# Performance work log

Hardware: AMD Instinct MI355X
Metric: run time of the kernel (lower is better)

## Reference

```python
import jax, jax.numpy as jnp
import numpy as np

BS, NQ, NC, NT = 64, 300, 10, 30
W_CLASS, W_BBOX, W_GIOU = 2.0, 5.0, 2.0


def cxcywh_to_xyxy(b):
    c, s = b[..., :2], b[..., 2:]
    return jnp.concatenate([c - 0.5 * s, c + 0.5 * s], axis=-1)


def _area(b):
    return (b[..., 2] - b[..., 0]) * (b[..., 3] - b[..., 1])


def giou_pairwise(a, b):
    # a: [N,4] xyxy, b: [M,4] xyxy -> [N,M]
    sum_area = _area(a)[:, None] + _area(b)[None, :]
    lt = jnp.maximum(a[:, None, :2], b[None, :, :2])
    rb = jnp.minimum(a[:, None, 2:], b[None, :, 2:])
    wh = jnp.clip(rb - lt, 0.0)
    inter = wh[..., 0] * wh[..., 1]
    union = sum_area - inter
    iou = inter / union
    ltc = jnp.minimum(a[:, None, :2], b[None, :, :2])
    rbc = jnp.maximum(a[:, None, 2:], b[None, :, 2:])
    whc = jnp.clip(rbc - ltc, 0.0)
    areac = whc[..., 0] * whc[..., 1]
    return iou - (areac - union) / areac


def giou_elementwise(a, b):
    # a, b: [N,4] xyxy -> [N]
    sum_area = _area(a) + _area(b)
    lt = jnp.maximum(a[..., :2], b[..., :2])
    rb = jnp.minimum(a[..., 2:], b[..., 2:])
    wh = jnp.clip(rb - lt, 0.0)
    inter = wh[..., 0] * wh[..., 1]
    union = sum_area - inter
    iou = inter / union
    ltc = jnp.minimum(a[..., :2], b[..., :2])
    rbc = jnp.maximum(a[..., 2:], b[..., 2:])
    whc = jnp.clip(rbc - ltc, 0.0)
    areac = whc[..., 0] * whc[..., 1]
    return iou - (areac - union) / areac


def hungarian(cost):
    # Exact rectangular assignment (Kuhn-Munkres with potentials), rows n <= cols m.
    # Returns (row_ind, col_ind) of the n matched pairs, equivalent to
    # scipy.optimize.linear_sum_assignment.
    n, m = cost.shape
    u = np.zeros(n + 1)
    v = np.zeros(m + 1)
    p = np.zeros(m + 1, dtype=np.int64)    # p[j] = row matched to col j (1-based)
    way = np.zeros(m + 1, dtype=np.int64)
    for i in range(1, n + 1):
        p[0] = i
        j0 = 0
        minv = np.full(m + 1, np.inf)
        used = np.zeros(m + 1, dtype=bool)
        while True:
            used[j0] = True
            i0 = p[j0]
            cur = cost[i0 - 1] - u[i0] - v[1:]
            mask = ~used[1:]
            better = mask & (cur < minv[1:])
            minv[1:] = np.where(better, cur, minv[1:])
            way[1:] = np.where(better, j0, way[1:])
            free = np.nonzero(mask)[0]
            j1 = free[np.argmin(minv[1:][free])] + 1
            delta = minv[j1]
            u[p[used]] += delta
            v[used] -= delta
            minv[~used] -= delta
            j0 = j1
            if p[j0] == 0:
                break
        while j0 != 0:
            j1 = way[j0]
            p[j0] = p[j1]
            j0 = j1
    rows = p[1:] - 1
    cols = np.arange(m)
    sel = rows >= 0
    return rows[sel], cols[sel]


def compute_match(pred_logits, pred_boxes, labels, boxes):
    # Mirrors @torch.no_grad() match(): build cost matrix on device, assign on host.
    bs, nq, _ = pred_logits.shape
    t = boxes.shape[1]
    out_prob = jax.nn.sigmoid(pred_logits).reshape(bs * nq, -1)
    out_bbox = pred_boxes.reshape(bs * nq, 4)
    tgt_ids = labels.reshape(-1)
    tgt_bbox = boxes.reshape(-1, 4)
    cost_class = -out_prob[:, tgt_ids]                                   # [bs*nq, bs*t]
    cost_bbox = jnp.sum(jnp.abs(out_bbox[:, None, :] - tgt_bbox[None, :, :]), -1)
    cost_giou = -giou_pairwise(cxcywh_to_xyxy(out_bbox), cxcywh_to_xyxy(tgt_bbox))
    C = W_BBOX * cost_bbox + W_CLASS * cost_class + W_GIOU * cost_giou
    C = np.asarray(jax.device_get(C), dtype=np.float64).reshape(bs, nq, bs * t)
    bidx, sidx, tidx = [], [], []
    for b in range(bs):
        block = C[b, :, b * t:(b + 1) * t]          # [nq, t]
        r, c = hungarian(block.T)                   # rows = targets, cols = queries
        bidx.extend([b] * len(c))
        sidx.extend(c.tolist())
        tidx.extend(r.tolist())
    return (np.asarray(bidx, np.int64), np.asarray(sidx, np.int64),
            np.asarray(tidx, np.int64))


def compute_loss(pred_logits, pred_boxes, labels, boxes, bidx, sidx, tidx):
    bs, nq, _ = pred_logits.shape
    num = max(1, len(bidx))
    target_classes = jnp.full((bs, nq), 10, dtype=jnp.int32)
    target_classes = target_classes.at[bidx, sidx].set(
        labels[bidx, tidx].astype(jnp.int32))
    onehot = jax.nn.one_hot(target_classes, 11, dtype=pred_logits.dtype)[..., :10]
    # sigmoid focal loss, alpha=0.25, gamma=2, reduction='sum'
    x, t = pred_logits, onehot
    p = jax.nn.sigmoid(x)
    ce = jnp.maximum(x, 0.0) - x * t + jnp.log1p(jnp.exp(-jnp.abs(x)))
    p_t = p * t + (1.0 - p) * (1.0 - t)
    alpha_t = 0.25 * t + 0.75 * (1.0 - t)
    loss_ce = jnp.sum(alpha_t * ce * (1.0 - p_t) ** 2) / num
    src_boxes = pred_boxes[bidx, sidx]
    tgt_boxes = boxes[bidx, tidx]
    loss_bbox = jnp.sum(jnp.abs(src_boxes - tgt_boxes)) / num
    g = giou_elementwise(cxcywh_to_xyxy(src_boxes), cxcywh_to_xyxy(tgt_boxes))
    loss_giou = jnp.sum(1.0 - g) / num
    return loss_ce + 5.0 * loss_bbox + 2.0 * loss_giou


def setup_inputs() -> dict:
    key = jax.random.key(0)
    k0, k1, k2, k3 = jax.random.split(key, 4)
    pred_logits = jax.random.normal(k0, (BS, NQ, NC), dtype=jnp.float32)
    pred_boxes = jax.random.uniform(k1, (BS, NQ, 4), dtype=jnp.float32)
    labels = jax.random.randint(k2, (BS, NT), 0, 10, dtype=jnp.int64)
    boxes = jax.random.uniform(k3, (BS, NT, 4), dtype=jnp.float32)
    return {"pred_logits": pred_logits, "pred_boxes": pred_boxes,
            "labels": labels, "boxes": boxes}


def reference(pred_logits, pred_boxes, labels, boxes):
    bidx, sidx, tidx = compute_match(pred_logits, pred_boxes, labels, boxes)
    return compute_loss(pred_logits, pred_boxes, labels, boxes, bidx, sidx, tidx)
```

## Files before the change

### kernel.cpp

```cpp
#include <hip/hip_runtime.h>
#include <math.h>

#define NQ 300
#define NQP 301
#define NT 30
#define NC 10
#define NTH 512
#define NWAVE 8
#define INFF 3.0e38f

__device__ __forceinline__ float sigf(float x){ return 1.0f/(1.0f + expf(-x)); }
__device__ __forceinline__ float softplusf(float x){ return fmaxf(x,0.0f) + log1pf(expf(-fabsf(x))); }
__device__ __forceinline__ float readlane_f(float v, int l){
  return __int_as_float(__builtin_amdgcn_readlane(__float_as_int(v), l));
}
__device__ __forceinline__ int readlane_i(int v, int l){
  return __builtin_amdgcn_readlane(v, l);
}

template<int CTRL,int RMASK>
__device__ __forceinline__ float dppmin_f(float x){
  int t = __builtin_amdgcn_update_dpp(0x7f800000, __float_as_int(x), CTRL, RMASK, 0xf, false);
  return fminf(x, __int_as_float(t));
}
template<int CTRL,int RMASK>
__device__ __forceinline__ unsigned dppmin_u(unsigned x){
  unsigned t = (unsigned)__builtin_amdgcn_update_dpp((int)0xFFFFFFFFu, (int)x, CTRL, RMASK, 0xf, false);
  return x < t ? x : t;
}
template<int CTRL,int RMASK>
__device__ __forceinline__ float dppadd_f(float x){
  int t = __builtin_amdgcn_update_dpp(0, __float_as_int(x), CTRL, RMASK, 0xf, false);
  return x + __int_as_float(t);
}
__device__ __forceinline__ void wave_argmin64(float v, unsigned idx, float &ov, int &oj){
  float x = v;
  x = dppmin_f<0x111,0xf>(x); x = dppmin_f<0x112,0xf>(x);
  x = dppmin_f<0x114,0xf>(x); x = dppmin_f<0x118,0xf>(x);
  x = dppmin_f<0x142,0xa>(x); x = dppmin_f<0x143,0xc>(x);
  float vmin = __int_as_float(__builtin_amdgcn_readlane(__float_as_int(x), 63));
  unsigned c = (v == vmin) ? idx : 0xFFFFFFFFu;
  c = dppmin_u<0x111,0xf>(c); c = dppmin_u<0x112,0xf>(c);
  c = dppmin_u<0x114,0xf>(c); c = dppmin_u<0x118,0xf>(c);
  c = dppmin_u<0x142,0xa>(c); c = dppmin_u<0x143,0xc>(c);
  oj = __builtin_amdgcn_readlane((int)c, 63);
  ov = vmin;
}
__device__ __forceinline__ float wave_sum64(float v){
  float x = v;
  x = dppadd_f<0x111,0xf>(x); x = dppadd_f<0x112,0xf>(x);
  x = dppadd_f<0x114,0xf>(x); x = dppadd_f<0x118,0xf>(x);
  x = dppadd_f<0x142,0xa>(x); x = dppadd_f<0x143,0xc>(x);
  return __int_as_float(__builtin_amdgcn_readlane(__float_as_int(x), 63));
}

__global__ __launch_bounds__(NTH) void hm_main(
    const float* __restrict__ logits,
    const float* __restrict__ pbox,
    const int*   __restrict__ labels,
    const float* __restrict__ tbox,
    float* __restrict__ out)
{
  const int b = blockIdx.x;
  const int tid = threadIdx.x;
  const int wv = tid >> 6, ln = tid & 63;

  __shared__ float D[NT*NQ];
  __shared__ float psmT[NC*NQP];
  __shared__ float traw[NT][4], txy[NT][4], tarea[NT];
  __shared__ int   tlab[NT];
  __shared__ float uu[NT+1];
  __shared__ int   pcol[NQ];
  __shared__ int   claimA[NQ];
  __shared__ int   rargm[NT];
  __shared__ float redw[NWAVE];

  const bool v4 = ln < (NQ - 256);

  float qcx[5],qcy[5],qw[5],qh[5],qx0[5],qy0[5],qx1[5],qy1[5],qar[5];
  {
    const float4* pb4 = (const float4*)pbox + (size_t)b*NQ;
    #pragma unroll
    for (int k = 0; k < 5; ++k) {
      float4 s = (k < 4 || v4) ? pb4[ln + (k<<6)] : make_float4(0.f,0.f,0.f,0.f);
      qcx[k]=s.x; qcy[k]=s.y; qw[k]=s.z; qh[k]=s.w;
      qx0[k]=s.x-0.5f*s.z; qy0[k]=s.y-0.5f*s.w;
      qx1[k]=s.x+0.5f*s.z; qy1[k]=s.y+0.5f*s.w;
      qar[k]=(qx1[k]-qx0[k])*(qy1[k]-qy0[k]);
    }
  }
  if (tid < NT) {
    float4 s = ((const float4*)tbox)[(size_t)b*NT + tid];
    traw[tid][0]=s.x; traw[tid][1]=s.y; traw[tid][2]=s.z; traw[tid][3]=s.w;
    float x0=s.x-0.5f*s.z, y0=s.y-0.5f*s.w, x1=s.x+0.5f*s.z, y1=s.y+0.5f*s.w;
    txy[tid][0]=x0; txy[tid][1]=y0; txy[tid][2]=x1; txy[tid][3]=y1;
    tarea[tid]=(x1-x0)*(y1-y0);
    tlab[tid]=labels[b*NT + tid];
  }
  for (int j = tid; j < NQ; j += NTH) { pcol[j]=0; claimA[j]=0x7fffffff; }

  float tot = 0.f;
  for (int e = tid; e < NQ*NC; e += NTH) {
    float x = logits[(size_t)b*NQ*NC + e];
    float pr = sigf(x);
    int q = e / NC, c = e - q*NC;
    psmT[c*NQP + q] = pr;
    tot += 0.75f * softplusf(x) * pr * pr;
  }
  __syncthreads();

  for (int i = wv; i < NT; i += NWAVE) {
    const float t0=traw[i][0], t1=traw[i][1], t2=traw[i][2], t3=traw[i][3];
    const float x0=txy[i][0], y0=txy[i][1], x1=txy[i][2], y1=txy[i][3];
    const float ta=tarea[i];
    const float* prow = &psmT[tlab[i]*NQP];
    float bv=INFF; unsigned bj=0xFFFFFFFFu;
    #pragma unroll
    for (int k = 0; k < 5; ++k) {
      if (k < 4 || v4) {
        int q = ln + (k<<6);
        float cb = fabsf(qcx[k]-t0)+fabsf(qcy[k]-t1)+fabsf(qw[k]-t2)+fabsf(qh[k]-t3);
        float lt0=fmaxf(qx0[k],x0), lt1=fmaxf(qy0[k],y0);
        float rb0=fminf(qx1[k],x1), rb1=fminf(qy1[k],y1);
        float iw=fmaxf(rb0-lt0,0.f), ih=fmaxf(rb1-lt1,0.f);
        float inter=iw*ih;
        float uni=qar[k]+ta-inter;
        float iou=inter/uni;
        float c0=fminf(qx0[k],x0), c1=fminf(qy0[k],y0);
        float c2=fmaxf(qx1[k],x1), c3=fmaxf(qy1[k],y1);
        float cw=fmaxf(c2-c0,0.f), ch=fmaxf(c3-c1,0.f);
        float areac=cw*ch;
        float g=iou-(areac-uni)/areac;
        float dval = 5.f*cb - 2.f*prow[q] - 2.f*g;
        D[i*NQ+q] = dval;
        if (dval < bv) { bv=dval; bj=(unsigned)q; }
      }
    }
    float vmin; int jmin;
    wave_argmin64(bv, bj, vmin, jmin);
    if (ln == 0) { uu[i+1]=vmin; rargm[i]=jmin; }
  }
  __syncthreads();

  if (wv == 0) {
    const int lane = ln;
    float u_reg = (lane < NT) ? uu[lane+1] : 0.f;
    float vv0=0.f,vv1=0.f,vv2=0.f,vv3=0.f,vv4=0.f;
    int jm = (lane < NT) ? rargm[lane] : 0;
    bool winner = false;
    if (lane < NT) {
      atomicMin(&claimA[jm], lane);
      winner = (claimA[jm] == lane);
      if (winner) pcol[jm] = lane + 1;
    }
    unsigned freerows = (unsigned)__ballot(lane < NT && !winner);
    int pc0=pcol[lane], pc1=pcol[lane+64], pc2=pcol[lane+128], pc3=pcol[lane+192];
    int pc4 = v4 ? pcol[lane+256] : 0;
    int wy0=0, wy1=0, wy2=0, wy3=0, wy4=0;

    while (freerows) {
      int fr = __builtin_ctz(freerows); freerows &= (freerows - 1);
      const int it = fr + 1;
      float mn0=INFF,mn1=INFF,mn2=INFF,mn3=INFF,mn4=INFF;
      int usedm = 0;
      bool onpath = (lane == fr);
      int j0 = -1, i0 = it, j1 = 0;
      for (;;) {
        float ui0 = readlane_f(u_reg, i0-1);
        const float* Drow = &D[(i0-1)*NQ];
        float lval = INFF; unsigned lidx = 0xFFFFFFFFu;
        #define SCAN_K(K, MN, VV, WY) \
          if ((K < 4 || v4) && !((usedm>>K)&1)) { \
            float cur = Drow[lane + (K<<6)] - ui0 - VV; \
            if (cur < MN) { MN = cur; WY = j0; } \
            if (MN < lval) { lval = MN; lidx = (unsigned)(lane + (K<<6)); } \
          }
        SCAN_K(0, mn0, vv0, wy0)
        SCAN_K(1, mn1, vv1, wy1)
        SCAN_K(2, mn2, vv2, wy2)
        SCAN_K(3, mn3, vv3, wy3)
        SCAN_K(4, mn4, vv4, wy4)
        #undef SCAN_K
        float delta; int j1i;
        wave_argmin64(lval, lidx, delta, j1i);
        j1 = j1i;
        if (onpath) u_reg += delta;
        #define UPD_K(K, MN, VV) if ((usedm>>K)&1) VV -= delta; else MN -= delta;
        UPD_K(0, mn0, vv0) UPD_K(1, mn1, vv1) UPD_K(2, mn2, vv2)
        UPD_K(3, mn3, vv3) UPD_K(4, mn4, vv4)
        #undef UPD_K
        int slot = j1 >> 6, src = j1 & 63;
        int pv;
        switch (slot) { case 0: pv=pc0; break; case 1: pv=pc1; break;
                        case 2: pv=pc2; break; case 3: pv=pc3; break; default: pv=pc4; }
        int pj1 = readlane_i(pv, src);
        if (pj1 == 0) break;
        onpath = onpath || (lane == (pj1-1));
        if (lane == src) usedm |= (1 << slot);
        j0 = j1; i0 = pj1;
      }
      int j = j1;
      for (;;) {
        int slot = j >> 6, src = j & 63;
        int wval;
        switch (slot) { case 0: wval=wy0; break; case 1: wval=wy1; break;
                        case 2: wval=wy2; break; case 3: wval=wy3; break; default: wval=wy4; }
        int jp = readlane_i(wval, src);
        int rr;
        if (jp < 0) rr = it;
        else {
          int s2 = jp >> 6, l2 = jp & 63;
          int pv2;
          switch (s2) { case 0: pv2=pc0; break; case 1: pv2=pc1; break;
                        case 2: pv2=pc2; break; case 3: pv2=pc3; break; default: pv2=pc4; }
          rr = readlane_i(pv2, l2);
        }
        switch (slot) {
          case 0: if (lane==src) pc0=rr; break;
          case 1: if (lane==src) pc1=rr; break;
          case 2: if (lane==src) pc2=rr; break;
          case 3: if (lane==src) pc3=rr; break;
          default: if (lane==src) pc4=rr; break;
        }
        if (jp < 0) break;
        j = jp;
      }
    }
    pcol[lane]=pc0; pcol[lane+64]=pc1; pcol[lane+128]=pc2; pcol[lane+192]=pc3;
    if (v4) pcol[lane+256]=pc4;
  }
  __syncthreads();

  if (wv < 5 && (wv < 4 || v4)) {
    int q = ln + (wv<<6);
    int row = pcol[q];
    if (row > 0) {
      int ti = row-1;
      float scx,scy,sw,sh,sx0,sy0,sx1,sy1,sar;
      switch (wv) {
        case 0: scx=qcx[0];scy=qcy[0];sw=qw[0];sh=qh[0];sx0=qx0[0];sy0=qy0[0];sx1=qx1[0];sy1=qy1[0];sar=qar[0]; break;
        case 1: scx=qcx[1];scy=qcy[1];sw=qw[1];sh=qh[1];sx0=qx0[1];sy0=qy0[1];sx1=qx1[1];sy1=qy1[1];sar=qar[1]; break;
        case 2: scx=qcx[2];scy=qcy[2];sw=qw[2];sh=qh[2];sx0=qx0[2];sy0=qy0[2];sx1=qx1[2];sy1=qy1[2];sar=qar[2]; break;
        case 3: scx=qcx[3];scy=qcy[3];sw=qw[3];sh=qh[3];sx0=qx0[3];sy0=qy0[3];sx1=qx1[3];sy1=qy1[3];sar=qar[3]; break;
        default: scx=qcx[4];scy=qcy[4];sw=qw[4];sh=qh[4];sx0=qx0[4];sy0=qy0[4];sx1=qx1[4];sy1=qy1[4];sar=qar[4]; break;
      }
      float l1 = fabsf(scx-traw[ti][0])+fabsf(scy-traw[ti][1])
               + fabsf(sw -traw[ti][2])+fabsf(sh -traw[ti][3]);
      float lt0=fmaxf(sx0,txy[ti][0]), lt1=fmaxf(sy0,txy[ti][1]);
      float rb0=fminf(sx1,txy[ti][2]), rb1=fminf(sy1,txy[ti][3]);
      float iw=fmaxf(rb0-lt0,0.f), ih=fmaxf(rb1-lt1,0.f);
      float inter=iw*ih;
      float uni=sar+tarea[ti]-inter;
      float iou=inter/uni;
      float c0=fminf(sx0,txy[ti][0]), c1=fminf(sy0,txy[ti][1]);
      float c2=fmaxf(sx1,txy[ti][2]), c3=fmaxf(sy1,txy[ti][3]);
      float cw=fmaxf(c2-c0,0.f), ch=fmaxf(c3-c1,0.f);
      float areac=cw*ch;
      float g=iou-(areac-uni)/areac;
      float x  = logits[((size_t)b*NQ+q)*NC + tlab[ti]];
      float pr = psmT[tlab[ti]*NQP + q];
      float sp = softplusf(x);
      tot += (0.25f*(sp - x)*(1.f-pr)*(1.f-pr) - 0.75f*sp*pr*pr) + 5.f*l1 + 2.f*(1.f-g);
    }
  }
  float wsum = wave_sum64(tot);
  if (ln == 0) redw[wv] = wsum;
  __syncthreads();
  if (tid == 0) {
    float s = 0.f;
    #pragma unroll
    for (int w = 0; w < NWAVE; ++w) s += redw[w];
    atomicAdd(out, s * (1.0f/1920.0f));
  }
}

extern "C" void kernel_launch(void* const* d_in, const int* in_sizes, int n_in,
                              void* d_out, int out_size, void* d_ws, size_t ws_size,
                              hipStream_t stream) {
  const float* logits = (const float*)d_in[0];
  const float* pbox   = (const float*)d_in[1];
  const int*   labels = (const int*)d_in[2];
  const float* tbox   = (const float*)d_in[3];
  hipMemsetAsync(d_out, 0, sizeof(float), stream);
  hm_main<<<dim3(64), dim3(NTH), 0, stream>>>(logits, pbox, labels, tbox, (float*)d_out);
}
```

Measured before the change: 28.65 us.

## Offload focal-loss background sum to extra blocks and vectorize logits loads

Launches 64 extra blocks that compute the all-negative focal-loss term over the logits and atomically add it to the output, so the main matching blocks only compute sigmoids for the cost table. Logits are now read as float4 in both paths. Precise expf/log1pf calls are replaced with fast __expf/__logf intrinsics. This shortens the critical path of the serial Hungarian blocks, but adds a second read of the logits, extra atomics and some loss of precision in softplus for large |x|.

```diff
diff --git a/kernel.cpp b/kernel.cpp
--- a/kernel.cpp
+++ b/kernel.cpp
@@ -9,8 +9,12 @@
 #define NWAVE 8
 #define INFF 3.0e38f
 
-__device__ __forceinline__ float sigf(float x){ return 1.0f/(1.0f + expf(-x)); }
-__device__ __forceinline__ float softplusf(float x){ return fmaxf(x,0.0f) + log1pf(expf(-fabsf(x))); }
+__device__ __forceinline__ float sigf(float x){ return 1.0f/(1.0f + __expf(-x)); }
+__device__ __forceinline__ float softplusf(float x){ return fmaxf(x,0.0f) + __logf(1.0f + __expf(-fabsf(x))); }
+__device__ __forceinline__ float focal0(float x){
+  float pr = sigf(x);
+  return 0.75f * softplusf(x) * pr * pr;
+}
 __device__ __forceinline__ float readlane_f(float v, int l){
   return __int_as_float(__builtin_amdgcn_readlane(__float_as_int(v), l));
 }
@@ -61,7 +65,7 @@
     const float* __restrict__ tbox,
     float* __restrict__ out)
 {
-  const int b = blockIdx.x;
+  const int bid = blockIdx.x;
   const int tid = threadIdx.x;
   const int wv = tid >> 6, ln = tid & 63;
 
@@ -75,6 +79,27 @@
   __shared__ int   rargm[NT];
   __shared__ float redw[NWAVE];
 
+  if (bid >= 64) {
+    const int b = bid - 64;
+    const float4* lg4 = (const float4*)(logits + (size_t)b*NQ*NC);
+    float tot = 0.f;
+    for (int e = tid; e < NQ*NC/4; e += NTH) {
+      float4 v = lg4[e];
+      tot += focal0(v.x) + focal0(v.y) + focal0(v.z) + focal0(v.w);
+    }
+    float wsum = wave_sum64(tot);
+    if (ln == 0) redw[wv] = wsum;
+    __syncthreads();
+    if (tid == 0) {
+      float s = 0.f;
+      #pragma unroll
+      for (int w = 0; w < NWAVE; ++w) s += redw[w];
+      atomicAdd(out, s * (1.0f/1920.0f));
+    }
+    return;
+  }
+
+  const int b = bid;
   const bool v4 = ln < (NQ - 256);
 
   float qcx[5],qcy[5],qw[5],qh[5],qx0[5],qy0[5],qx1[5],qy1[5],qar[5];
@@ -99,13 +124,18 @@
   }
   for (int j = tid; j < NQ; j += NTH) { pcol[j]=0; claimA[j]=0x7fffffff; }
 
-  float tot = 0.f;
-  for (int e = tid; e < NQ*NC; e += NTH) {
-    float x = logits[(size_t)b*NQ*NC + e];
-    float pr = sigf(x);
-    int q = e / NC, c = e - q*NC;
-    psmT[c*NQP + q] = pr;
-    tot += 0.75f * softplusf(x) * pr * pr;
+  {
+    const float4* lg4 = (const float4*)(logits + (size_t)b*NQ*NC);
+    for (int e4 = tid; e4 < NQ*NC/4; e4 += NTH) {
+      float4 v = lg4[e4];
+      int e = e4 << 2;
+      #pragma unroll
+      for (int j = 0; j < 4; ++j) {
+        float x = (j==0)?v.x:(j==1)?v.y:(j==2)?v.z:v.w;
+        int ee = e + j, q = ee / NC, c = ee - q*NC;
+        psmT[c*NQP + q] = sigf(x);
+      }
+    }
   }
   __syncthreads();
 
@@ -231,6 +261,7 @@
   }
   __syncthreads();
 
+  float tot = 0.f;
   if (wv < 5 && (wv < 4 || v4)) {
     int q = ln + (wv<<6);
     int row = pcol[q];
@@ -282,5 +313,5 @@
   const int*   labels = (const int*)d_in[2];
   const float* tbox   = (const float*)d_in[3];
   hipMemsetAsync(d_out, 0, sizeof(float), stream);
-  hm_main<<<dim3(64), dim3(NTH), 0, stream>>>(logits, pbox, labels, tbox, (float*)d_out);
-}
+  hm_main<<<dim3(128), dim3(NTH), 0, stream>>>(logits, pbox, labels, tbox, (float*)d_out);
+}
```

Result: faster. 24.82 us (-13.4%).
